# Kernel optimization log

Measured on AMD Instinct MI355X. Metric: run time of the kernel, lower is better.

## Reference

```python
import jax, jax.numpy as jnp
import numpy as np
from jax import lax


def setup_inputs() -> dict:
    key = jax.random.key(0)
    ks = jax.random.split(key, 16)
    f32 = jnp.float32
    g = lambda k, shp, s=0.02: jax.random.normal(k, shp, dtype=f32) * s
    inp = {
        "x": jax.random.normal(ks[0], (4, 1, 4096), dtype=f32),
        # conv_time: Conv1d(1,128,3,pad=1)
        "conv_time_w": g(ks[1], (128, 1, 3)), "conv_time_b": jnp.zeros((128,), f32),
        "bn0_g": jnp.ones((128,), f32), "bn0_b": jnp.zeros((128,), f32),
        "bn0_m": jnp.zeros((128,), f32), "bn0_v": jnp.ones((128,), f32),
        # block1: Conv1d(128,256,3,pad=1)+BN
        "conv1_w": g(ks[2], (256, 128, 3)), "conv1_b": jnp.zeros((256,), f32),
        "bn1_g": jnp.ones((256,), f32), "bn1_b": jnp.zeros((256,), f32),
        "bn1_m": jnp.zeros((256,), f32), "bn1_v": jnp.ones((256,), f32),
        # block2: Conv1d(256,512,3,pad=1)+BN
        "conv2_w": g(ks[3], (512, 256, 3)), "conv2_b": jnp.zeros((512,), f32),
        "bn2_g": jnp.ones((512,), f32), "bn2_b": jnp.zeros((512,), f32),
        "bn2_m": jnp.zeros((512,), f32), "bn2_v": jnp.ones((512,), f32),
        # GAT 1: fc Linear(512,512), attn_fc Linear(1024,1)
        "gat1_fc_w": g(ks[4], (512, 512)), "gat1_fc_b": jnp.zeros((512,), f32),
        "gat1_attn_w": g(ks[5], (1024,)), "gat1_attn_b": jnp.zeros((), f32),
        # GAT 2: fc Linear(512,256), attn_fc Linear(512,1)
        "gat2_fc_w": g(ks[6], (256, 512)), "gat2_fc_b": jnp.zeros((256,), f32),
        "gat2_attn_w": g(ks[7], (512,)), "gat2_attn_b": jnp.zeros((), f32),
        # head: Linear(256,2)
        "fc_w": g(ks[8], (2, 256)), "fc_b": jnp.zeros((2,), f32),
    }
    return inp


def _conv1d(x, w, b):
    # x: [B,C,T], w: [O,C,3], padding=1
    y = lax.conv_general_dilated(x, w, window_strides=(1,), padding=((1, 1),),
                                 dimension_numbers=("NCH", "OIH", "NCH"))
    return y + b[None, :, None]


def _bn(x, g, b, m, v):
    # eval-mode BatchNorm1d over channel dim
    return (x - m[None, :, None]) * (g * lax.rsqrt(v + 1e-5))[None, :, None] + b[None, :, None]


def _maxpool2(x):
    return lax.reduce_window(x, -jnp.inf, lax.max, (1, 1, 2), (1, 1, 2), "VALID")


def _gat(x2d, fc_w, fc_b, aw, ab):
    # Faithful to: cat([h_i, h_j]) @ attn_w == h_i @ aw[:d] + h_j @ aw[d:]
    h = x2d @ fc_w.T + fc_b           # [N, d]
    d = h.shape[-1]
    s1 = h @ aw[:d]                   # [N] (query part, h.repeat(1,N))
    s2 = h @ aw[d:]                   # [N] (key part,   h.repeat(N,1))
    e = jax.nn.leaky_relu(s1[:, None] + s2[None, :] + ab, negative_slope=0.01)  # [N,N]
    att = jax.nn.softmax(e, axis=1)
    return att @ h                    # [N, d]


def reference(x, conv_time_w, conv_time_b, bn0_g, bn0_b, bn0_m, bn0_v,
              conv1_w, conv1_b, bn1_g, bn1_b, bn1_m, bn1_v,
              conv2_w, conv2_b, bn2_g, bn2_b, bn2_m, bn2_v,
              gat1_fc_w, gat1_fc_b, gat1_attn_w, gat1_attn_b,
              gat2_fc_w, gat2_fc_b, gat2_attn_w, gat2_attn_b,
              fc_w, fc_b):
    h = jax.nn.relu(_bn(_conv1d(x, conv_time_w, conv_time_b), bn0_g, bn0_b, bn0_m, bn0_v))
    h = _maxpool2(jax.nn.relu(_bn(_conv1d(h, conv1_w, conv1_b), bn1_g, bn1_b, bn1_m, bn1_v)))
    h = _maxpool2(jax.nn.relu(_bn(_conv1d(h, conv2_w, conv2_b), bn2_g, bn2_b, bn2_m, bn2_v)))
    h = jnp.transpose(h, (0, 2, 1))   # [B, S, 512]
    B, S, C = h.shape
    g = h.reshape(B * S, C)           # whole batch flattened into one graph (as in source)
    g = _gat(g, gat1_fc_w, gat1_fc_b, gat1_attn_w, gat1_attn_b)   # [N, 512]
    g = _gat(g, gat2_fc_w, gat2_fc_b, gat2_attn_w, gat2_attn_b)   # [N, 256]
    pooled = g.reshape(B, S, -1).mean(axis=1)                     # [B, 256]
    return pooled @ fc_w.T + fc_b     # [B, 2] (dropout is identity in eval)
```

## Files before the change

kernel.cpp:

```cpp
#include <hip/hip_runtime.h>
#include <hip/hip_bf16.h>
#include <math.h>


#define NN 4096
#define BB 4
#define TT0 4096

__global__ void k_conv_time2(const float* __restrict__ x, const float* __restrict__ w,
                             const float* __restrict__ cb, const float* __restrict__ g,
                             const float* __restrict__ bbp, const float* __restrict__ m,
                             const float* __restrict__ v, float* __restrict__ out) {
  int gid = blockIdx.x * 256 + threadIdx.x;
  int t4 = gid & 1023;
  int o = (gid >> 10) & 127;
  int b = gid >> 17;
  int t = t4 * 4;
  float sc = g[o] * rsqrtf(v[o] + 1e-5f);
  float sh = (cb[o] - m[o]) * sc + bbp[o];
  const float* xb = x + b * 4096;
  float4 xc = *(const float4*)&xb[t];
  float xm = (t > 0) ? xb[t - 1] : 0.f;
  float xp = (t + 4 < 4096) ? xb[t + 4] : 0.f;
  const float* wo = w + o * 3;
  float w0 = wo[0], w1 = wo[1], w2 = wo[2];
  float4 y;
  y.x = fmaxf((w0 * xm   + w1 * xc.x + w2 * xc.y) * sc + sh, 0.f);
  y.y = fmaxf((w0 * xc.x + w1 * xc.y + w2 * xc.z) * sc + sh, 0.f);
  y.z = fmaxf((w0 * xc.y + w1 * xc.z + w2 * xc.w) * sc + sh, 0.f);
  y.w = fmaxf((w0 * xc.z + w1 * xc.w + w2 * xp  ) * sc + sh, 0.f);
  *(float4*)&out[((size_t)(b * 128) + o) * 4096 + t] = y;
}

template <int C, int TIN>
__global__ __launch_bounds__(256, 4)
void k_conv_pool5(const float* __restrict__ in, const float* __restrict__ w,
                  const float* __restrict__ cb, const float* __restrict__ g,
                  const float* __restrict__ bbp, const float* __restrict__ m,
                  const float* __restrict__ v, float* __restrict__ out, int OCH) {
  constexpr int TOUT = TIN / 2;
  constexpr int CC = 32;
  __shared__ float xs[CC][68];
  __shared__ float wsh[CC][196];

  int bx = blockIdx.x;
  int nT = TIN / 64;
  int tb = bx % nT;
  int ob = (bx / nT) % (OCH / 64);
  int b  = bx / (nT * (OCH / 64));
  int tid = threadIdx.x;
  int tg = tid & 15, og = tid >> 4;

  float acc[4][4];
  #pragma unroll
  for (int i = 0; i < 4; i++)
    #pragma unroll
    for (int p = 0; p < 4; p++) acc[i][p] = 0.f;

  int t0 = tb * 64;
  const float* wbase = w + (size_t)(ob * 64) * C * 3;

  for (int c0 = 0; c0 < C; c0 += CC) {
    for (int e = tid; e < CC * 66; e += 256) {
      int cc = e / 66, tl = e - cc * 66;
      int t = t0 - 1 + tl;
      xs[cc][tl] = (t >= 0 && t < TIN) ? in[((size_t)(b * C) + c0 + cc) * TIN + t] : 0.f;
    }
    for (int e = tid; e < CC * 192; e += 256) {
      int oo = e / 96, r = e - oo * 96;
      int cc = r / 3, k = r - cc * 3;
      wsh[cc][oo * 3 + k] = wbase[(size_t)oo * C * 3 + (size_t)c0 * 3 + r];
    }
    __syncthreads();
    #pragma unroll 8
    for (int cc = 0; cc < CC; ++cc) {
      float4 xa = *(const float4*)&xs[cc][4 * tg];
      float x4 = xs[cc][4 * tg + 4];
      float x5 = xs[cc][4 * tg + 5];
      float xv[6] = {xa.x, xa.y, xa.z, xa.w, x4, x5};
      float4 wa = *(const float4*)&wsh[cc][og * 12];
      float4 wb = *(const float4*)&wsh[cc][og * 12 + 4];
      float4 wc = *(const float4*)&wsh[cc][og * 12 + 8];
      float wv[12] = {wa.x, wa.y, wa.z, wa.w, wb.x, wb.y, wb.z, wb.w, wc.x, wc.y, wc.z, wc.w};
      #pragma unroll
      for (int oi = 0; oi < 4; oi++)
        #pragma unroll
        for (int p = 0; p < 4; p++)
          acc[oi][p] += wv[oi * 3] * xv[p] + wv[oi * 3 + 1] * xv[p + 1]
                      + wv[oi * 3 + 2] * xv[p + 2];
    }
    __syncthreads();
  }

  #pragma unroll
  for (int oi = 0; oi < 4; oi++) {
    int o = ob * 64 + og * 4 + oi;
    float sc = g[o] * rsqrtf(v[o] + 1e-5f);
    float sh = (cb[o] - m[o]) * sc + bbp[o];
    float y0 = fmaxf(acc[oi][0] * sc + sh, acc[oi][1] * sc + sh);
    float y1 = fmaxf(acc[oi][2] * sc + sh, acc[oi][3] * sc + sh);
    float2 r;
    r.x = fmaxf(y0, 0.f);
    r.y = fmaxf(y1, 0.f);
    *(float2*)&out[((size_t)(b * OCH) + o) * TOUT + tb * 32 + 2 * tg] = r;
  }
}

__global__ __launch_bounds__(512, 1)
void k_gemm_chw(const float* __restrict__ A, const float* __restrict__ Wt,
                const float* __restrict__ bias, float* __restrict__ Cout) {
  constexpr int K = 512, N = 512;
  __shared__ float As[32][132];
  __shared__ float Bs[32][68];
  int i0 = blockIdx.x * 128, j0 = blockIdx.y * 64;
  int tid = threadIdx.x;
  int tx = tid & 15, ty = tid >> 4;
  int b = i0 >> 10, s0 = i0 & 1023;
  const float* Ab = A + (size_t)b * K * 1024 + s0;

  float acc[4][4];
  #pragma unroll
  for (int ii = 0; ii < 4; ii++)
    #pragma unroll
    for (int jj = 0; jj < 4; jj++) acc[ii][jj] = 0.f;

  int ka = (tid + 0) >> 5, i4a = tid & 31;
  int kb = (tid + 512) >> 5, i4b = tid & 31;
  float4 pa0, pa1; float pb[4];

  pa0 = *(const float4*)&Ab[(size_t)ka * 1024 + 4 * i4a];
  pa1 = *(const float4*)&Ab[(size_t)kb * 1024 + 4 * i4b];
  #pragma unroll
  for (int r = 0; r < 4; r++) {
    int e = tid + 512 * r; int j = e >> 5, k = e & 31;
    pb[r] = Wt[(size_t)(j0 + j) * K + k];
  }

  for (int kt = 0; kt < K; kt += 32) {
    *(float4*)&As[ka][4 * i4a] = pa0;
    *(float4*)&As[kb][4 * i4b] = pa1;
    #pragma unroll
    for (int r = 0; r < 4; r++) {
      int e = tid + 512 * r; int j = e >> 5, k = e & 31;
      Bs[k][j] = pb[r];
    }
    __syncthreads();
    int ktn = (kt + 32 < K) ? kt + 32 : 0;
    float4 na0 = *(const float4*)&Ab[(size_t)(ktn + ka) * 1024 + 4 * i4a];
    float4 na1 = *(const float4*)&Ab[(size_t)(ktn + kb) * 1024 + 4 * i4b];
    float nb[4];
    #pragma unroll
    for (int r = 0; r < 4; r++) {
      int e = tid + 512 * r; int j = e >> 5, k = e & 31;
      nb[r] = Wt[(size_t)(j0 + j) * K + ktn + k];
    }
    #pragma unroll 4
    for (int kk = 0; kk < 32; ++kk) {
      float4 a4 = *(const float4*)&As[kk][ty * 4];
      float4 b4 = *(const float4*)&Bs[kk][tx * 4];
      float a[4] = {a4.x, a4.y, a4.z, a4.w};
      float bv[4] = {b4.x, b4.y, b4.z, b4.w};
      #pragma unroll
      for (int ii = 0; ii < 4; ii++)
        #pragma unroll
        for (int jj = 0; jj < 4; jj++) acc[ii][jj] += a[ii] * bv[jj];
    }
    __syncthreads();
    pa0 = na0; pa1 = na1;
    #pragma unroll
    for (int r = 0; r < 4; r++) pb[r] = nb[r];
  }

  float4 bias4 = *(const float4*)&bias[j0 + 4 * tx];
  #pragma unroll
  for (int ii = 0; ii < 4; ii++) {
    int i = i0 + ty * 4 + ii;
    float4 o4;
    o4.x = acc[ii][0] + bias4.x; o4.y = acc[ii][1] + bias4.y;
    o4.z = acc[ii][2] + bias4.z; o4.w = acc[ii][3] + bias4.w;
    *(float4*)&Cout[(size_t)i * N + j0 + 4 * tx] = o4;
  }
}

__global__ __launch_bounds__(256, 2)
void k_gemm_rm(const float* __restrict__ A, const float* __restrict__ Wt,
               const float* __restrict__ bias, float* __restrict__ Cout) {
  constexpr int K = 512, N = 256;
  __shared__ float As[32][68];
  __shared__ float Bs[32][68];
  int i0 = blockIdx.x * 64, j0 = blockIdx.y * 64;
  int tid = threadIdx.x;
  int tx = tid & 15, ty = tid >> 4;

  float acc[4][4];
  #pragma unroll
  for (int ii = 0; ii < 4; ii++)
    #pragma unroll
    for (int jj = 0; jj < 4; jj++) acc[ii][jj] = 0.f;

  float4 pa[2]; float pb[8];
  #pragma unroll
  for (int r = 0; r < 2; r++) {
    int e4 = tid + 256 * r; int i = e4 >> 3, k4 = e4 & 7;
    pa[r] = *(const float4*)&A[(size_t)(i0 + i) * K + 4 * k4];
  }
  #pragma unroll
  for (int r = 0; r < 8; r++) {
    int e = tid + 256 * r; int j = e >> 5, k = e & 31;
    pb[r] = Wt[(size_t)(j0 + j) * K + k];
  }

  for (int kt = 0; kt < K; kt += 32) {
    #pragma unroll
    for (int r = 0; r < 2; r++) {
      int e4 = tid + 256 * r; int i = e4 >> 3, k4 = e4 & 7;
      As[4 * k4 + 0][i] = pa[r].x; As[4 * k4 + 1][i] = pa[r].y;
      As[4 * k4 + 2][i] = pa[r].z; As[4 * k4 + 3][i] = pa[r].w;
    }
    #pragma unroll
    for (int r = 0; r < 8; r++) {
      int e = tid + 256 * r; int j = e >> 5, k = e & 31;
      Bs[k][j] = pb[r];
    }
    __syncthreads();
    int ktn = (kt + 32 < K) ? kt + 32 : 0;
    float4 na[2]; float nb[8];
    #pragma unroll
    for (int r = 0; r < 2; r++) {
      int e4 = tid + 256 * r; int i = e4 >> 3, k4 = e4 & 7;
      na[r] = *(const float4*)&A[(size_t)(i0 + i) * K + ktn + 4 * k4];
    }
    #pragma unroll
    for (int r = 0; r < 8; r++) {
      int e = tid + 256 * r; int j = e >> 5, k = e & 31;
      nb[r] = Wt[(size_t)(j0 + j) * K + ktn + k];
    }
    #pragma unroll 4
    for (int kk = 0; kk < 32; ++kk) {
      float4 a4 = *(const float4*)&As[kk][ty * 4];
      float4 b4 = *(const float4*)&Bs[kk][tx * 4];
      float a[4] = {a4.x, a4.y, a4.z, a4.w};
      float bv[4] = {b4.x, b4.y, b4.z, b4.w};
      #pragma unroll
      for (int ii = 0; ii < 4; ii++)
        #pragma unroll
        for (int jj = 0; jj < 4; jj++) acc[ii][jj] += a[ii] * bv[jj];
    }
    __syncthreads();
    pa[0] = na[0]; pa[1] = na[1];
    #pragma unroll
    for (int r = 0; r < 8; r++) pb[r] = nb[r];
  }

  float4 bias4 = *(const float4*)&bias[j0 + 4 * tx];
  #pragma unroll
  for (int ii = 0; ii < 4; ii++) {
    int i = i0 + ty * 4 + ii;
    float4 o4;
    o4.x = acc[ii][0] + bias4.x; o4.y = acc[ii][1] + bias4.y;
    o4.z = acc[ii][2] + bias4.z; o4.w = acc[ii][3] + bias4.w;
    *(float4*)&Cout[(size_t)i * N + j0 + 4 * tx] = o4;
  }
}

template <int D>
__global__ void k_rowdot(const float* __restrict__ h, const float* __restrict__ aw,
                         float* __restrict__ s1, float* __restrict__ s2,
                         int* __restrict__ rnk) {
  if (blockIdx.x < 16) rnk[blockIdx.x * 256 + threadIdx.x] = 0;
  int wid = threadIdx.x >> 6, lane = threadIdx.x & 63;
  int i = blockIdx.x * 4 + wid;
  const float* hr = h + (size_t)i * D;
  float d1 = 0.f, d2 = 0.f;
  #pragma unroll
  for (int d = lane; d < D; d += 64) {
    float hv = hr[d];
    d1 += hv * aw[d];
    d2 += hv * aw[D + d];
  }
  for (int off = 32; off; off >>= 1) {
    d1 += __shfl_down(d1, off, 64);
    d2 += __shfl_down(d2, off, 64);
  }
  if (lane == 0) { s1[i] = d1; s2[i] = d2; }
}

__global__ void k_rank(const float* __restrict__ s2v, int* __restrict__ rnk) {
  __shared__ float ls[1024];
  int j = blockIdx.x * 256 + threadIdx.x;
  int base = blockIdx.y * 1024;
  float vj = s2v[j];
  for (int e = threadIdx.x; e < 1024; e += 256) ls[e] = s2v[base + e];
  __syncthreads();
  int cnt = 0;
  #pragma unroll 8
  for (int r = 0; r < 1024; ++r) {
    float vr = ls[r];
    cnt += (vr < vj || (vr == vj && (base + r) < j)) ? 1 : 0;
  }
  atomicAdd(&rnk[j], cnt);
}

__global__ void k_scatter(const float* __restrict__ s2v, const int* __restrict__ rnk,
                          float* __restrict__ svals, int* __restrict__ sidx) {
  int j = blockIdx.x * 256 + threadIdx.x;
  int r = rnk[j];
  svals[r] = s2v[j];
  sidx[r] = j;
}

__global__ void k_tw(const float* __restrict__ s1, const float* __restrict__ svals,
                     const float* __restrict__ abp, int* __restrict__ tarr,
                     float* __restrict__ Aarr, float* __restrict__ Barr,
                     float* __restrict__ wp, float* __restrict__ wm) {
  int i = blockIdx.x * 256 + threadIdx.x;
  float ab = abp[0], M2 = svals[NN - 1];
  float alpha = s1[i] + ab;
  float cthr = -alpha;
  int lo = 0, hi = NN;
  while (lo < hi) {
    int mid = (lo + hi) >> 1;
    if (svals[mid] < cthr) lo = mid + 1; else hi = mid;
  }
  tarr[i] = lo;
  float e1 = alpha + M2;
  float gam = fmaxf(e1, 0.01f * e1);
  Aarr[i] = expf(e1 - gam);
  Barr[i] = expf(0.01f * e1 - gam);
  float d = svals[i] - M2;
  wp[i] = expf(d);
  wm[i] = expf(0.01f * d);
}

__global__ void k_scan_den(const float* __restrict__ wp, const float* __restrict__ wm,
                           float* __restrict__ preden, float* __restrict__ sufden) {
  __shared__ float csP[256], csM[256];
  int tid = threadIdx.x;
  int base = tid * 16;
  float sm = 0.f, sp = 0.f;
  for (int u = 0; u < 16; u++) { sm += wm[base + u]; sp += wp[base + u]; }
  csM[tid] = sm; csP[tid] = sp;
  __syncthreads();
  float offM = 0.f;
  for (int c = 0; c < tid; c++) offM += csM[c];
  float offP = 0.f;
  for (int c = tid + 1; c < 256; c++) offP += csP[c];
  float run = offM;
  for (int u = 0; u < 16; u++) { preden[base + u] = run; run += wm[base + u]; }
  if (tid == 255) preden[NN] = run;
  float runp = offP;
  if (tid == 255) sufden[NN] = 0.f;
  for (int u = 15; u >= 0; u--) { runp += wp[base + u]; sufden[base + u] = runp; }
}

template <int D>
__global__ void k_chunksum(const float* __restrict__ h, const int* __restrict__ sidx,
                           const float* __restrict__ wp, const float* __restrict__ wm,
                           float* __restrict__ csP, float* __restrict__ csM) {
  constexpr int CPT = D / 256;
  int c = blockIdx.x, tid = threadIdx.x;
  __shared__ int lidx[32];
  __shared__ float lwp[32], lwm[32];
  if (tid < 32) {
    int r = c * 32 + tid;
    lidx[tid] = sidx[r]; lwp[tid] = wp[r]; lwm[tid] = wm[r];
  }
  __syncthreads();
  float aP[CPT], aM[CPT];
  #pragma unroll
  for (int q = 0; q < CPT; q++) { aP[q] = 0.f; aM[q] = 0.f; }
  for (int u = 0; u < 32; u++) {
    const float* hr = h + (size_t)lidx[u] * D;
    float fp = lwp[u], fm = lwm[u];
    #pragma unroll
    for (int q = 0; q < CPT; q++) {
      float hv = hr[tid + q * 256];
      aP[q] += fp * hv; aM[q] += fm * hv;
    }
  }
  #pragma unroll
  for (int q = 0; q < CPT; q++) {
    csP[(size_t)c * D + tid + q * 256] = aP[q];
    csM[(size_t)c * D + tid + q * 256] = aM[q];
  }
}

template <int D>
__global__ void k_chunkoff(const float* __restrict__ csP, const float* __restrict__ csM,
                           float* __restrict__ offP, float* __restrict__ offM) {
  int d = blockIdx.x * 256 + threadIdx.x;
  float rm = 0.f;
  for (int cb = 0; cb < 128; cb += 16) {
    float vals[16];
    #pragma unroll
    for (int u = 0; u < 16; u++) vals[u] = csM[(size_t)(cb + u) * D + d];
    #pragma unroll
    for (int u = 0; u < 16; u++) { offM[(size_t)(cb + u) * D + d] = rm; rm += vals[u]; }
  }
  float rp = 0.f;
  for (int cb = 127; cb >= 15; cb -= 16) {
    float vals[16];
    #pragma unroll
    for (int u = 0; u < 16; u++) vals[u] = csP[(size_t)(cb - u) * D + d];
    #pragma unroll
    for (int u = 0; u < 16; u++) { offP[(size_t)(cb - u) * D + d] = rp; rp += vals[u]; }
  }
}

template <int D>
__global__ void k_scanwrite(const float* __restrict__ h, const int* __restrict__ sidx,
                            const float* __restrict__ wp, const float* __restrict__ wm,
                            const float* __restrict__ offP, const float* __restrict__ offM,
                            float* __restrict__ Pre, float* __restrict__ Suf) {
  constexpr int CPT = D / 256;
  int c = blockIdx.x, tid = threadIdx.x;
  __shared__ int lidx[32];
  __shared__ float lwp[32], lwm[32];
  if (tid < 32) {
    int r = c * 32 + tid;
    lidx[tid] = sidx[r]; lwp[tid] = wp[r]; lwm[tid] = wm[r];
  }
  __syncthreads();
  float runM[CPT], runP[CPT];
  #pragma unroll
  for (int q = 0; q < CPT; q++) {
    int d = tid + q * 256;
    runM[q] = offM[(size_t)c * D + d];
    runP[q] = offP[(size_t)c * D + d];
  }
  for (int u = 0; u < 32; u++) {
    const float* hr = h + (size_t)lidx[u] * D;
    float fm = lwm[u];
    #pragma unroll
    for (int q = 0; q < CPT; q++) {
      int d = tid + q * 256;
      Pre[(size_t)(c * 32 + u) * D + d] = runM[q];
      runM[q] += fm * hr[d];
    }
  }
  if (c == 127) {
    #pragma unroll
    for (int q = 0; q < CPT; q++) Pre[(size_t)NN * D + tid + q * 256] = runM[q];
    #pragma unroll
    for (int q = 0; q < CPT; q++) Suf[(size_t)NN * D + tid + q * 256] = 0.f;
  }
  for (int u = 31; u >= 0; u--) {
    const float* hr = h + (size_t)lidx[u] * D;
    float fp = lwp[u];
    #pragma unroll
    for (int q = 0; q < CPT; q++) {
      int d = tid + q * 256;
      runP[q] += fp * hr[d];
      Suf[(size_t)(c * 32 + u) * D + d] = runP[q];
    }
  }
}

template <int D>
__global__ void k_apply(const float* __restrict__ Pre, const float* __restrict__ Suf,
                        const float* __restrict__ preden, const float* __restrict__ sufden,
                        const int* __restrict__ tarr, const float* __restrict__ Aarr,
                        const float* __restrict__ Barr, float* __restrict__ outg) {
  int i = blockIdx.x;
  int t = tarr[i];
  float A = Aarr[i], Bv = Barr[i];
  float den = A * sufden[t] + Bv * preden[t];
  float inv = 1.f / den;
  const float* Pr = Pre + (size_t)t * D;
  const float* Sr = Suf + (size_t)t * D;
  for (int d = threadIdx.x; d < D; d += 256)
    outg[(size_t)i * D + d] = (A * Sr[d] + Bv * Pr[d]) * inv;
}

__global__ void k_pool(const float* __restrict__ g2, float* __restrict__ pp) {
  int b = blockIdx.x >> 4, ch = blockIdx.x & 15;
  const float* base = g2 + ((size_t)(b * 1024) + ch * 64) * 256 + threadIdx.x;
  float s = 0.f;
  for (int r = 0; r < 64; r++) s += base[(size_t)r * 256];
  pp[(size_t)blockIdx.x * 256 + threadIdx.x] = s;
}

__global__ void k_head2(const float* __restrict__ pp, const float* __restrict__ fcw,
                        const float* __restrict__ fcb, float* __restrict__ out) {
  __shared__ float pooled[4][256];
  int tid = threadIdx.x;
  for (int b = 0; b < 4; b++) {
    float s = 0.f;
    for (int ch = 0; ch < 16; ch++) s += pp[(size_t)(b * 16 + ch) * 256 + tid];
    pooled[b][tid] = s * (1.f / 1024.f);
  }
  __syncthreads();
  if (tid < 8) {
    int b = tid >> 1, c = tid & 1;
    float acc = fcb[c];
    for (int cc = 0; cc < 256; cc++) acc += pooled[b][cc] * fcw[c * 256 + cc];
    out[b * 2 + c] = acc;
  }
}

extern "C" void kernel_launch(void* const* d_in, const int* in_sizes, int n_in,
                              void* d_out, int out_size, void* d_ws, size_t ws_size,
                              hipStream_t stream) {
  const float* x    = (const float*)d_in[0];
  const float* ctw  = (const float*)d_in[1];
  const float* ctb  = (const float*)d_in[2];
  const float* bn0g = (const float*)d_in[3];
  const float* bn0b = (const float*)d_in[4];
  const float* bn0m = (const float*)d_in[5];
  const float* bn0v = (const float*)d_in[6];
  const float* c1w  = (const float*)d_in[7];
  const float* c1b  = (const float*)d_in[8];
  const float* bn1g = (const float*)d_in[9];
  const float* bn1b = (const float*)d_in[10];
  const float* bn1m = (const float*)d_in[11];
  const float* bn1v = (const float*)d_in[12];
  const float* c2w  = (const float*)d_in[13];
  const float* c2b  = (const float*)d_in[14];
  const float* bn2g = (const float*)d_in[15];
  const float* bn2b = (const float*)d_in[16];
  const float* bn2m = (const float*)d_in[17];
  const float* bn2v = (const float*)d_in[18];
  const float* g1w  = (const float*)d_in[19];
  const float* g1b  = (const float*)d_in[20];
  const float* g1aw = (const float*)d_in[21];
  const float* g1ab = (const float*)d_in[22];
  const float* g2w  = (const float*)d_in[23];
  const float* g2b  = (const float*)d_in[24];
  const float* g2aw = (const float*)d_in[25];
  const float* g2ab = (const float*)d_in[26];
  const float* fcw  = (const float*)d_in[27];
  const float* fcb  = (const float*)d_in[28];
  float* ws = (float*)d_ws;

  const size_t SLOT = (size_t)(NN + 1) * 512;
  float* slot0 = ws;
  float* slot1 = ws + SLOT;
  float* slot2 = ws + 2 * SLOT;
  float* slot3 = ws + 3 * SLOT;
  float* sm    = ws + 4 * SLOT;
  float* s1    = sm;
  float* s2    = sm + 4096;
  float* svals = sm + 8192;
  int*   sidx  = (int*)(sm + 12288);
  int*   tarr  = (int*)(sm + 16384);
  float* Aarr  = sm + 20480;
  float* Barr  = sm + 24576;
  float* wp    = sm + 28672;
  float* wm    = sm + 32768;
  float* preden = sm + 36864;
  float* sufden = sm + 40968;
  float* csP   = sm + 45072;
  float* csM   = csP + 65536;
  float* offP  = csM + 65536;
  float* offM  = offP + 65536;
  int*   rnk   = (int*)(offM + 65536);
  float* pp    = offM + 65536 + 4096;

  k_conv_time2<<<BB * 128 * 1024 / 256, 256, 0, stream>>>(x, ctw, ctb, bn0g, bn0b, bn0m, bn0v, slot0);
  k_conv_pool5<128, 4096><<<BB * 4 * 64, 256, 0, stream>>>(
      slot0, c1w, c1b, bn1g, bn1b, bn1m, bn1v, slot1, 256);
  k_conv_pool5<256, 2048><<<BB * 8 * 32, 256, 0, stream>>>(
      slot1, c2w, c2b, bn2g, bn2b, bn2m, bn2v, slot2, 512);

  k_gemm_chw<<<dim3(32, 8), 512, 0, stream>>>(slot2, g1w, g1b, slot3);
  k_rowdot<512><<<NN / 4, 256, 0, stream>>>(slot3, g1aw, s1, s2, rnk);
  k_rank<<<dim3(16, 4), 256, 0, stream>>>(s2, rnk);
  k_scatter<<<16, 256, 0, stream>>>(s2, rnk, svals, sidx);
  k_tw<<<NN / 256, 256, 0, stream>>>(s1, svals, g1ab, tarr, Aarr, Barr, wp, wm);
  k_scan_den<<<1, 256, 0, stream>>>(wp, wm, preden, sufden);
  k_chunksum<512><<<128, 256, 0, stream>>>(slot3, sidx, wp, wm, csP, csM);
  k_chunkoff<512><<<2, 256, 0, stream>>>(csP, csM, offP, offM);
  k_scanwrite<512><<<128, 256, 0, stream>>>(slot3, sidx, wp, wm, offP, offM, slot1, slot0);
  k_apply<512><<<NN, 256, 0, stream>>>(slot1, slot0, preden, sufden, tarr, Aarr, Barr, slot2);

  k_gemm_rm<<<dim3(64, 4), 256, 0, stream>>>(slot2, g2w, g2b, slot3);
  k_rowdot<256><<<NN / 4, 256, 0, stream>>>(slot3, g2aw, s1, s2, rnk);
  k_rank<<<dim3(16, 4), 256, 0, stream>>>(s2, rnk);
  k_scatter<<<16, 256, 0, stream>>>(s2, rnk, svals, sidx);
  k_tw<<<NN / 256, 256, 0, stream>>>(s1, svals, g2ab, tarr, Aarr, Barr, wp, wm);
  k_scan_den<<<1, 256, 0, stream>>>(wp, wm, preden, sufden);
  k_chunksum<256><<<128, 256, 0, stream>>>(slot3, sidx, wp, wm, csP, csM);
  k_chunkoff<256><<<1, 256, 0, stream>>>(csP, csM, offP, offM);
  k_scanwrite<256><<<128, 256, 0, stream>>>(slot3, sidx, wp, wm, offP, offM, slot1, slot0);
  k_apply<256><<<NN, 256, 0, stream>>>(slot1, slot0, preden, sufden, tarr, Aarr, Barr, slot2);

  k_pool<<<BB * 16, 256, 0, stream>>>(slot2, pp);
  k_head2<<<1, 256, 0, stream>>>(pp, fcw, fcb, (float*)d_out);
}
```

Before: 426.7 us.

## Retile conv+pool kernel: wave-uniform weights from global, wider time tile

```diff
diff --git a/kernel.cpp b/kernel.cpp
--- a/kernel.cpp
+++ b/kernel.cpp
@@ -34,22 +34,23 @@
 
 template <int C, int TIN>
 __global__ __launch_bounds__(256, 4)
-void k_conv_pool5(const float* __restrict__ in, const float* __restrict__ w,
+void k_conv_pool7(const float* __restrict__ in, const float* __restrict__ w,
                   const float* __restrict__ cb, const float* __restrict__ g,
                   const float* __restrict__ bbp, const float* __restrict__ m,
                   const float* __restrict__ v, float* __restrict__ out, int OCH) {
   constexpr int TOUT = TIN / 2;
   constexpr int CC = 32;
-  __shared__ float xs[CC][68];
-  __shared__ float wsh[CC][196];
+  __shared__ float xs[CC][264];
 
   int bx = blockIdx.x;
-  int nT = TIN / 64;
+  int nT = TIN / 256;
   int tb = bx % nT;
-  int ob = (bx / nT) % (OCH / 64);
-  int b  = bx / (nT * (OCH / 64));
+  int ob = (bx / nT) % (OCH / 16);
+  int b  = bx / (nT * (OCH / 16));
   int tid = threadIdx.x;
-  int tg = tid & 15, og = tid >> 4;
+  int lane = tid & 63;
+  int wv = __builtin_amdgcn_readfirstlane(tid >> 6);
+  int t0 = tb * 256;
 
   float acc[4][4];
   #pragma unroll
@@ -57,52 +58,59 @@
     #pragma unroll
     for (int p = 0; p < 4; p++) acc[i][p] = 0.f;
 
-  int t0 = tb * 64;
-  const float* wbase = w + (size_t)(ob * 64) * C * 3;
+  const float* wq = w + (size_t)(ob * 16 + wv * 4) * C * 3;
 
   for (int c0 = 0; c0 < C; c0 += CC) {
-    for (int e = tid; e < CC * 66; e += 256) {
-      int cc = e / 66, tl = e - cc * 66;
-      int t = t0 - 1 + tl;
-      xs[cc][tl] = (t >= 0 && t < TIN) ? in[((size_t)(b * C) + c0 + cc) * TIN + t] : 0.f;
-    }
-    for (int e = tid; e < CC * 192; e += 256) {
-      int oo = e / 96, r = e - oo * 96;
-      int cc = r / 3, k = r - cc * 3;
-      wsh[cc][oo * 3 + k] = wbase[(size_t)oo * C * 3 + (size_t)c0 * 3 + r];
+    for (int u = 0; u < 9; u++) {
+      int e4 = tid + 256 * u;
+      if (e4 < CC * 66) {
+        int cc = e4 / 66, j4 = e4 - cc * 66;
+        int t = t0 - 4 + 4 * j4;
+        const float* src = &in[((size_t)(b * C) + c0 + cc) * TIN + t];
+        float4 val;
+        if (t >= 0 && t + 3 < TIN) {
+          val = *(const float4*)src;
+        } else {
+          val.x = (t     >= 0 && t     < TIN) ? src[0] : 0.f;
+          val.y = (t + 1 >= 0 && t + 1 < TIN) ? src[1] : 0.f;
+          val.z = (t + 2 >= 0 && t + 2 < TIN) ? src[2] : 0.f;
+          val.w = (t + 3 >= 0 && t + 3 < TIN) ? src[3] : 0.f;
+        }
+        *(float4*)&xs[cc][4 * j4] = val;
+      }
     }
     __syncthreads();
-    #pragma unroll 8
+    #pragma unroll 4
     for (int cc = 0; cc < CC; ++cc) {
-      float4 xa = *(const float4*)&xs[cc][4 * tg];
-      float x4 = xs[cc][4 * tg + 4];
-      float x5 = xs[cc][4 * tg + 5];
-      float xv[6] = {xa.x, xa.y, xa.z, xa.w, x4, x5};
-      float4 wa = *(const float4*)&wsh[cc][og * 12];
-      float4 wb = *(const float4*)&wsh[cc][og * 12 + 4];
-      float4 wc = *(const float4*)&wsh[cc][og * 12 + 8];
-      float wv[12] = {wa.x, wa.y, wa.z, wa.w, wb.x, wb.y, wb.z, wb.w, wc.x, wc.y, wc.z, wc.w};
+      float w0[4], w1[4], w2[4];
+      #pragma unroll
+      for (int oi = 0; oi < 4; oi++) {
+        const float* wr = wq + ((size_t)oi * C + c0 + cc) * 3;
+        w0[oi] = wr[0]; w1[oi] = wr[1]; w2[oi] = wr[2];
+      }
+      float2 xl = *(const float2*)&xs[cc][4 * lane + 2];
+      float4 xc = *(const float4*)&xs[cc][4 * lane + 4];
+      float2 xr = *(const float2*)&xs[cc][4 * lane + 8];
+      float xv[6] = {xl.y, xc.x, xc.y, xc.z, xc.w, xr.x};
       #pragma unroll
       for (int oi = 0; oi < 4; oi++)
         #pragma unroll
         for (int p = 0; p < 4; p++)
-          acc[oi][p] += wv[oi * 3] * xv[p] + wv[oi * 3 + 1] * xv[p + 1]
-                      + wv[oi * 3 + 2] * xv[p + 2];
+          acc[oi][p] += w0[oi] * xv[p] + w1[oi] * xv[p + 1] + w2[oi] * xv[p + 2];
     }
     __syncthreads();
   }
 
+  int base_o = ob * 16 + wv * 4;
   #pragma unroll
   for (int oi = 0; oi < 4; oi++) {
-    int o = ob * 64 + og * 4 + oi;
+    int o = base_o + oi;
     float sc = g[o] * rsqrtf(v[o] + 1e-5f);
     float sh = (cb[o] - m[o]) * sc + bbp[o];
-    float y0 = fmaxf(acc[oi][0] * sc + sh, acc[oi][1] * sc + sh);
-    float y1 = fmaxf(acc[oi][2] * sc + sh, acc[oi][3] * sc + sh);
     float2 r;
-    r.x = fmaxf(y0, 0.f);
-    r.y = fmaxf(y1, 0.f);
-    *(float2*)&out[((size_t)(b * OCH) + o) * TOUT + tb * 32 + 2 * tg] = r;
+    r.x = fmaxf(fmaxf(acc[oi][0] * sc + sh, acc[oi][1] * sc + sh), 0.f);
+    r.y = fmaxf(fmaxf(acc[oi][2] * sc + sh, acc[oi][3] * sc + sh), 0.f);
+    *(float2*)&out[((size_t)(b * OCH) + o) * TOUT + tb * 128 + 2 * lane] = r;
   }
 }
 
@@ -557,9 +565,9 @@
   float* pp    = offM + 65536 + 4096;
 
   k_conv_time2<<<BB * 128 * 1024 / 256, 256, 0, stream>>>(x, ctw, ctb, bn0g, bn0b, bn0m, bn0v, slot0);
-  k_conv_pool5<128, 4096><<<BB * 4 * 64, 256, 0, stream>>>(
+  k_conv_pool7<128, 4096><<<BB * 16 * 16, 256, 0, stream>>>(
       slot0, c1w, c1b, bn1g, bn1b, bn1m, bn1v, slot1, 256);
-  k_conv_pool5<256, 2048><<<BB * 8 * 32, 256, 0, stream>>>(
+  k_conv_pool7<256, 2048><<<BB * 32 * 8, 256, 0, stream>>>(
       slot1, c2w, c2b, bn2g, bn2b, bn2m, bn2v, slot2, 512);
 
   k_gemm_chw<<<dim3(32, 8), 512, 0, stream>>>(slot2, g1w, g1b, slot3);
```

Result: faster. 403.6 us (-5.4%).
